# Kernel tuning notes

Hardware: AMD Instinct MI355X
Metric: run time of the kernel (lower is better)

Reference implementation:

```python
import jax, jax.numpy as jnp
import numpy as np

EPS_BN = 1e-5
K_DET = 50

def conv2d(x, w, b, pad):
    y = jax.lax.conv_general_dilated(x, w, (1, 1), [(pad, pad), (pad, pad)],
                                     dimension_numbers=('NCHW', 'OIHW', 'NCHW'))
    return y + b[None, :, None, None]

def branch2(x, w1, b1, w2, b2):
    # conv3x3 -> relu -> conv1x1
    return conv2d(jax.nn.relu(conv2d(x, w1, b1, 1)), w2, b2, 0)

def roi_head(x, w1, b1, g, beta, m, v, w2, b2):
    # conv3x3 -> BN(eval) -> relu -> global avg pool -> conv1x1
    h = conv2d(x, w1, b1, 1)
    h = (h - m[None, :, None, None]) * (g[None, :, None, None] / jnp.sqrt(v[None, :, None, None] + EPS_BN)) + beta[None, :, None, None]
    h = jax.nn.relu(h)
    h = jnp.mean(h, axis=(2, 3), keepdims=True)
    return conv2d(h, w2, b2, 0)[:, :, 0, 0]

def nms_hm(heat, kernel=3):
    pad = (kernel - 1) // 2
    hmax = jax.lax.reduce_window(heat, -jnp.inf, jax.lax.max,
                                 (1, 1, kernel, kernel), (1, 1, 1, 1),
                                 [(0, 0), (0, 0), (pad, pad), (pad, pad)])
    return heat * (hmax == heat).astype(heat.dtype)

def select_topk(heat, K):
    B, C, H, W = heat.shape
    s_all, i_all = jax.lax.top_k(heat.reshape(B, C, H * W), K)   # per-class topk
    scores, idx = jax.lax.top_k(s_all.reshape(B, C * K), K)      # overall topk
    classes = idx // K
    inds = jnp.take_along_axis(i_all.reshape(B, C * K), idx, axis=1)  # flat HW inds
    return scores, inds, classes

def roi_align_7x7(feat, boxes, sr=2):
    # torchvision roi_align, spatial_scale=1, aligned=False, sampling_ratio=sr
    B, C, H, W = feat.shape
    N = boxes.shape[0]
    b = boxes[:, 0].astype(jnp.int32)
    x1, y1, x2, y2 = boxes[:, 1], boxes[:, 2], boxes[:, 3], boxes[:, 4]
    roi_w = jnp.maximum(x2 - x1, 1.0)
    roi_h = jnp.maximum(y2 - y1, 1.0)
    bw = roi_w / 7.0
    bh = roi_h / 7.0
    S = 7 * sr
    off = (jnp.arange(S, dtype=feat.dtype) + 0.5) / sr  # sample offsets in bin units
    xs = x1[:, None] + bw[:, None] * off[None, :]       # (N,S)
    ys = y1[:, None] + bh[:, None] * off[None, :]
    X = jnp.broadcast_to(xs[:, None, :], (N, S, S))
    Y = jnp.broadcast_to(ys[:, :, None], (N, S, S))
    valid = (X > -1.0) & (X < W) & (Y > -1.0) & (Y < H)
    Xc = jnp.clip(X, 0.0, W - 1.0)
    Yc = jnp.clip(Y, 0.0, H - 1.0)
    x0 = jnp.floor(Xc).astype(jnp.int32)
    y0 = jnp.floor(Yc).astype(jnp.int32)
    x1i = jnp.minimum(x0 + 1, W - 1)
    y1i = jnp.minimum(y0 + 1, H - 1)
    lx = Xc - x0
    ly = Yc - y0
    flat = feat.transpose(0, 2, 3, 1).reshape(B * H * W, C)
    base = (b * H * W)[:, None, None]
    g = lambda yy, xx: flat[base + yy * W + xx]  # (N,S,S,C)
    v = (((1 - ly) * (1 - lx))[..., None] * g(y0, x0)
         + ((1 - ly) * lx)[..., None] * g(y0, x1i)
         + (ly * (1 - lx))[..., None] * g(y1i, x0)
         + (ly * lx)[..., None] * g(y1i, x1i))
    v = v * valid[..., None]
    v = v.reshape(N, 7, sr, 7, sr, C).mean(axis=(2, 4))
    return v.transpose(0, 3, 1, 2)  # (N,C,7,7)

def project_to_rect(calib, pts):
    c_u, c_v = calib[:, 0, 2], calib[:, 1, 2]
    f_u, f_v = calib[:, 0, 0], calib[:, 1, 1]
    b_x = calib[:, 0, 3] / (-f_u)
    b_y = calib[:, 1, 3] / (-f_v)
    x = (pts[:, 0] - c_u) * pts[:, 2] / f_u + b_x
    y = (pts[:, 1] - c_v) * pts[:, 2] / f_v + b_y
    return jnp.stack([x, y, pts[:, 2]], -1)

HEAD_NAMES = ['dep', 'o3', 's3', 'hd']

def setup_inputs():
    key = jax.random.key(0)
    ks = iter(jax.random.split(key, 64))
    B, Cin, H, W = 8, 64, 96, 320
    HC, NC = 256, 3
    f32 = jnp.float32
    rn = lambda shape, s=0.02: s * jax.random.normal(next(ks), shape, f32)
    inp = {}
    inp['features'] = jax.random.normal(next(ks), (B, Cin, H, W), f32)
    base = jnp.array([[700., 0., 640., 0.], [0., 700., 192., 0.], [0., 0., 1., 0.]], f32)
    inp['calib'] = base[None] + (jax.random.uniform(next(ks), (B, 3, 4), f32) - 0.5) * 2.0
    crb = jnp.array([[0., 0.], [1280., 384.]], f32)
    inp['coord_ranges'] = crb[None] + (jax.random.uniform(next(ks), (B, 2, 2), f32) - 0.5) * 2.0
    inp['mean_size'] = jnp.array([[3.88, 1.63, 1.53], [0.84, 0.66, 1.76], [1.76, 0.60, 1.73]], f32)
    inp['hm_w1'] = rn((HC, Cin, 3, 3)); inp['hm_b1'] = jnp.zeros(HC, f32)
    inp['hm_w2'] = rn((3, HC, 1, 1)); inp['hm_b2'] = jnp.full((3,), -np.log(1 / 0.1 - 1), f32)
    inp['o2_w1'] = rn((HC, Cin, 3, 3)); inp['o2_b1'] = jnp.zeros(HC, f32)
    inp['o2_w2'] = rn((2, HC, 1, 1)); inp['o2_b2'] = jnp.zeros(2, f32)
    inp['s2_w1'] = rn((HC, Cin, 3, 3)); inp['s2_b1'] = jnp.zeros(HC, f32)
    inp['s2_w2'] = rn((2, HC, 1, 1)); inp['s2_b2'] = 8.0 * jnp.ones(2, f32)
    Croi = Cin + 2 + NC
    for name, oc in zip(HEAD_NAMES, [2, 2, 4, 24]):
        inp[name + '_w1'] = rn((HC, Croi, 3, 3)); inp[name + '_b1'] = jnp.zeros(HC, f32)
        inp[name + '_g'] = 1.0 + 0.1 * jax.random.normal(next(ks), (HC,), f32)
        inp[name + '_beta'] = 0.1 * jax.random.normal(next(ks), (HC,), f32)
        inp[name + '_m'] = 0.1 * jax.random.normal(next(ks), (HC,), f32)
        inp[name + '_v'] = 1.0 + jax.random.uniform(next(ks), (HC,), f32)
        inp[name + '_w2'] = rn((oc, HC, 1, 1)); inp[name + '_b2'] = jnp.zeros(oc, f32)
    return inp

def reference(features, calib, coord_ranges, mean_size,
              hm_w1, hm_b1, hm_w2, hm_b2,
              o2_w1, o2_b1, o2_w2, o2_b2,
              s2_w1, s2_b1, s2_w2, s2_b2,
              dep_w1, dep_b1, dep_g, dep_beta, dep_m, dep_v, dep_w2, dep_b2,
              o3_w1, o3_b1, o3_g, o3_beta, o3_m, o3_v, o3_w2, o3_b2,
              s3_w1, s3_b1, s3_g, s3_beta, s3_m, s3_v, s3_w2, s3_b2,
              hd_w1, hd_b1, hd_g, hd_beta, hd_m, hd_v, hd_w2, hd_b2):
    B, Cf, H, W = features.shape
    dt = features.dtype
    heatmap = branch2(features, hm_w1, hm_b1, hm_w2, hm_b2)    # (B,3,H,W)
    offset_2d = branch2(features, o2_w1, o2_b1, o2_w2, o2_b2)  # (B,2,H,W)
    size_2d = branch2(features, s2_w1, s2_b1, s2_w2, s2_b2)    # (B,2,H,W)
    heat = nms_hm(heatmap)
    _, inds, classes = select_topk(heat, K_DET)                # (B,K)
    # coord map and box2d maps (B,5,H,W): [batch_idx, x1,y1,x2,y2]
    xs = jnp.arange(W, dtype=dt)
    ys = jnp.arange(H, dtype=dt)
    coord = jnp.stack([jnp.broadcast_to(xs[None, :], (H, W)),
                       jnp.broadcast_to(ys[:, None], (H, W))], 0)[None]
    center = coord + offset_2d
    bidx = jnp.broadcast_to(jnp.arange(B, dtype=dt)[:, None, None, None], (B, 1, H, W))
    box2d_maps = jnp.concatenate([bidx, center - size_2d / 2, center + size_2d / 2], 1)
    bm = box2d_maps.reshape(B, 5, H * W).transpose(0, 2, 1)    # (B,HW,5)
    boxes = jnp.take_along_axis(bm, inds[:, :, None], axis=1).reshape(-1, 5)  # (N,5)
    N = boxes.shape[0]
    roi_feat = roi_align_7x7(features, boxes)                  # (N,C,7,7)
    rb = boxes[:, 0].astype(jnp.int32)
    cr = coord_ranges[rb]                                      # (N,2,2)
    sx = cr[:, 1, 0] - cr[:, 0, 0]
    sy = cr[:, 1, 1] - cr[:, 0, 1]
    box_img = jnp.stack([boxes[:, 0],
                         boxes[:, 1] / W * sx + cr[:, 0, 0],
                         boxes[:, 2] / H * sy + cr[:, 0, 1],
                         boxes[:, 3] / W * sx + cr[:, 0, 0],
                         boxes[:, 4] / H * sy + cr[:, 0, 1]], -1)
    roi_calib = calib[rb]                                      # (N,3,4)
    ones = jnp.ones((N, 1), dt)
    p1 = project_to_rect(roi_calib, jnp.concatenate([box_img[:, 1:3], ones], -1))[:, :2]
    p2 = project_to_rect(roi_calib, jnp.concatenate([box_img[:, 3:5], ones], -1))[:, :2]
    t = jnp.arange(7, dtype=dt) / 6.0
    cx = p1[:, 0:1] + t[None, :] * (p2[:, 0:1] - p1[:, 0:1])   # (N,7)
    cy = p1[:, 1:2] + t[None, :] * (p2[:, 1:2] - p1[:, 1:2])
    coord_maps = jnp.stack([jnp.broadcast_to(cx[:, None, :], (N, 7, 7)),
                            jnp.broadcast_to(cy[:, :, None], (N, 7, 7))], 1)
    cls = classes.reshape(-1)
    NC = mean_size.shape[0]
    cls_hot = jax.nn.one_hot(cls, NC, dtype=dt)
    roi_in = jnp.concatenate([roi_feat, coord_maps,
                              jnp.broadcast_to(cls_hot[:, :, None, None], (N, NC, 7, 7))], 1)
    box2d_h = jnp.maximum(box_img[:, 4] - box_img[:, 2], 1.0)
    s3 = roi_head(roi_in, s3_w1, s3_b1, s3_g, s3_beta, s3_m, s3_v, s3_w2, s3_b2)  # (N,4)
    h3d_log_std = s3[:, 3:4]
    size3d_offset = s3[:, :3]
    size_3d = mean_size[cls] + size3d_offset
    f_u = roi_calib[:, 0, 0]
    depth_geo = size_3d[:, 0] / box2d_h * f_u
    dep = roi_head(roi_in, dep_w1, dep_b1, dep_g, dep_beta, dep_m, dep_v, dep_w2, dep_b2)
    depth_geo_log_std = (h3d_log_std[:, 0] + 2.0 * (jnp.log(f_u) - jnp.log(box2d_h)))[:, None]
    depth_log_std = jax.nn.logsumexp(jnp.concatenate([dep[:, 1:2], depth_geo_log_std], -1), axis=-1, keepdims=True)
    depth = jnp.concatenate([1.0 / (jax.nn.sigmoid(dep[:, 0:1]) + 1e-6) - 1.0 + depth_geo[:, None],
                             depth_log_std], -1)
    heading = roi_head(roi_in, hd_w1, hd_b1, hd_g, hd_beta, hd_m, hd_v, hd_w2, hd_b2)
    offset_3d = roi_head(roi_in, o3_w1, o3_b1, o3_g, o3_beta, o3_m, o3_v, o3_w2, o3_b2)
    return (heatmap, offset_2d, size_2d, heading, depth, offset_3d, size3d_offset, h3d_log_std)
```

## Files before the change

kernel.cpp:

```cpp
#include <hip/hip_runtime.h>
#include <math.h>

typedef unsigned short u16;
typedef unsigned int   u32;
typedef unsigned long long u64;
typedef __attribute__((ext_vector_type(8))) short short8;
typedef __attribute__((ext_vector_type(4))) float f32x4;

__device__ __forceinline__ float b2f(u16 v) { return __uint_as_float(((u32)v) << 16); }
__device__ __forceinline__ u16 f2b(float f) {
    u32 u = __float_as_uint(f);
    u32 r = (u + 0x7FFFu + ((u >> 16) & 1u)) >> 16;
    return (u16)r;
}
__device__ __forceinline__ float gload(const void* p, long i, int bf) {
    return bf ? b2f(((const u16*)p)[i]) : ((const float*)p)[i];
}
__device__ __forceinline__ void gstore(void* p, long i, float v, int bf) {
    if (bf) ((u16*)p)[i] = f2b(v);
    else    ((float*)p)[i] = v;
}

__device__ __forceinline__ u64 packKey(float v, int idx) {
    u32 u = __float_as_uint(v);
    u32 m = (u & 0x80000000u) ? ~u : (u | 0x80000000u);
    return ((u64)(~m) << 32) | (u32)idx;
}

__device__ int blockFlag(const void* feat) {
    __shared__ int fcnt;
    if (threadIdx.x == 0) fcnt = 0;
    __syncthreads();
    int sane = 0;
    for (int i = threadIdx.x; i < 512; i += blockDim.x) {
        u16 v = ((const u16*)feat)[i];
        float f = b2f(v);
        u32 e = (v >> 7) & 0xFF;
        float a = fabsf(f);
        sane += (e != 0xFF) && (f == 0.f || (a >= 1e-8f && a <= 1e4f));
    }
    atomicAdd(&fcnt, sane);
    __syncthreads();
    return fcnt >= 480;
}

#define BATCH 8
#define CIN   64
#define FH    96
#define FW    320
#define KDET  50
#define NROI  400
#define CROI  69
#define HW    (FH*FW)
#define CHUNK 1920
#define NCHUNK 16

#define WS_HEAT 0L
#define WS_OFF2 737280L
#define WS_SIZ2 1228800L
#define WS_NH   1720320L
#define WS_S1S  2457600L
#define WS_S1I  2458800L
#define WS_CLS  2460000L
#define WS_BOX  2460400L
#define WS_ROI  2462400L
#define WS_HOUT 3814800L
#define WS_W1T  3827600L
#define WS_WB16 3975056L
#define WS_W1H  4269968L
#define WS_PAR  4905872L
#define WS_FLAG 4938960L
#define WS_FEATT 4938964L
#define WS_END  (WS_FEATT + 7864320L)

#define PB_CAL 0
#define PB_CRN 96
#define PB_MSZ 128
#define PB_BR0 144
#define PB_HD0 3264

#define O_HEAT 0L
#define O_OFF2 737280L
#define O_SIZ2 1228800L
#define O_HEAD 1720320L
#define O_DEP  1729920L
#define O_OFF3 1730720L
#define O_S3D  1731520L
#define O_H3D  1732720L

struct WPtrs { const void* bw[3]; const void* hw[4]; };
struct Seg { const void* src; int n; int dst; };
struct Segs { Seg s[40]; int cnt; };

__global__ void kPrepWP(WPtrs P, Segs S, const void* __restrict__ feat,
                        int* __restrict__ flag, float* __restrict__ w1t,
                        u16* __restrict__ wb16, u16* __restrict__ whb,
                        float* __restrict__ par) {
    const int bf = blockFlag(feat);
    if (blockIdx.x == 0 && threadIdx.x == 0) *flag = bf;
    if (blockIdx.x < 5760) {
        int idx = blockIdx.x * 256 + threadIdx.x;
        if (idx < 147456) {
            int k = idx >> 8, c = idx & 255;
            w1t[idx] = gload(P.bw[0], (long)c * 576 + k, bf);
        } else if (idx < 589824) {
            int j = idx - 147456;
            int br = j / 147456, rem = j % 147456;
            int tap = rem / 16384;
            int r2 = rem & 16383;
            int s = r2 >> 13;
            int n = (r2 >> 5) & 255;
            int c5 = r2 & 31;
            int ci = s * 32 + c5;
            wb16[j] = f2b(gload(P.bw[br], (long)n * 576 + ci * 9 + tap, bf));
        } else {
            int j = idx - 589824;
            int h = j / 221184, rem = j % 221184;
            int tap = rem / 24576, rem2 = rem % 24576;
            int cs = rem2 / 8192, rem3 = rem2 % 8192;
            int oc = rem3 >> 5, jj = rem3 & 31;
            int ci = cs * 32 + jj;
            u16 val = 0;
            if (ci < CROI) val = f2b(gload(P.hw[h], (long)oc * 621 + ci * 9 + tap, bf));
            whb[j] = val;
        }
    } else {
        int sidx = blockIdx.x - 5760;
        if (sidx < S.cnt) {
            Seg sg = S.s[sidx];
            for (int i = threadIdx.x; i < sg.n; i += 256)
                par[sg.dst + i] = gload(sg.src, i, bf);
        }
    }
}

__global__ __launch_bounds__(256)
void kTrans(const void* __restrict__ feat, const int* __restrict__ flag,
            u16* __restrict__ featT) {
    __shared__ u16 t_lds[64][72];
    const int bf = *flag;
    const int x0 = blockIdx.x * 64, y = blockIdx.y, b = blockIdx.z;
    const int tid = threadIdx.x;
    for (int i = tid; i < 64 * 64; i += 256) {
        int c = i >> 6, x = i & 63;
        t_lds[x][c] = f2b(gload(feat, ((long)(b * CIN + c) * FH + y) * FW + x0 + x, bf));
    }
    __syncthreads();
    u16* outp = featT + (((long)b * FH + y) * FW + x0) * 64;
    for (int i = tid; i < 64 * 64; i += 256) {
        int x = i >> 6, c = i & 63;
        outp[(long)x * 64 + c] = t_lds[x][c];
    }
}

union MLds {
    struct { u16 a[4][68][72]; float red[8][64][3]; } c;
    struct {
        float in[4][3][36];
        union { float w[36 * 256]; float part[32 * 3 * 32]; } u;
    } s;
};

__global__ __launch_bounds__(512, 4)
void kBranch3M(const void* __restrict__ feat, const int* __restrict__ flag,
               const u16* __restrict__ wbAll,
               const float* __restrict__ bpAll,
               const float* __restrict__ w1t,
               void* __restrict__ outb, float* __restrict__ wsbase) {
    __shared__ __align__(16) MLds L;

    const long obase[3] = {O_HEAT, O_OFF2, O_SIZ2};
    const long wfs[3]   = {WS_HEAT, WS_OFF2, WS_SIZ2};

    const int bfl = *flag;
    const int tid = threadIdx.x;

    if (blockIdx.z == 8) {
        const int sidx = blockIdx.y * 5 + blockIdx.x;
        const int x0 = (sidx % 10) * 32;
        const int srem = sidx / 10;
        const int y = srem % 3;
        const int b = srem / 3;
        const float* bp = bpAll;
        const int OC = 3;
        const int xg = tid & 7, cg = tid >> 3;
        const int c0 = (cg & 31) * 8;

        float acc[8][4];
#pragma unroll
        for (int i = 0; i < 8; ++i)
#pragma unroll
            for (int j = 0; j < 4; ++j) acc[i][j] = 0.f;

        for (int chunk = 0; chunk < 16; ++chunk) {
            const int ci0 = chunk * 4;
            __syncthreads();
            for (int i = tid; i < 4 * 3 * 36; i += 512) {
                int xx = i % 36, t2 = i / 36;
                int r = t2 % 3, ci = t2 / 3;
                int gx = x0 - 1 + xx, gy = y - 1 + r;
                float v = 0.f;
                if (gx >= 0 && gx < FW && gy >= 0 && gy < FH)
                    v = gload(feat, ((long)(b * CIN + ci0 + ci) * FH + gy) * FW + gx, bfl);
                L.s.in[ci][r][xx] = v;
            }
            {
                const float4* src = (const float4*)(w1t + (long)ci0 * 9 * 256);
                float4* dst = (float4*)L.s.u.w;
                for (int i = tid; i < 36 * 256 / 4; i += 512) dst[i] = src[i];
            }
            __syncthreads();
            if (tid < 256) {
#pragma unroll
                for (int ci = 0; ci < 4; ++ci) {
#pragma unroll
                    for (int ky = 0; ky < 3; ++ky) {
                        const float* rowp = &L.s.in[ci][ky][xg * 4];
                        float inv[6];
                        *(float4*)&inv[0] = *(const float4*)&rowp[0];
                        *(float2*)&inv[4] = *(const float2*)&rowp[4];
#pragma unroll
                        for (int kx = 0; kx < 3; ++kx) {
                            const float* wp = &L.s.u.w[(ci * 9 + ky * 3 + kx) * 256 + c0];
                            float wv[8];
                            *(float4*)&wv[0] = *(const float4*)&wp[0];
                            *(float4*)&wv[4] = *(const float4*)&wp[4];
#pragma unroll
                            for (int cc = 0; cc < 8; ++cc)
#pragma unroll
                                for (int xx = 0; xx < 4; ++xx)
                                    acc[cc][xx] = fmaf(wv[cc], inv[xx + kx], acc[cc][xx]);
                        }
                    }
                }
            }
        }

        if (tid < 256) {
#pragma unroll
            for (int cc = 0; cc < 8; ++cc) {
                float b1v = bp[c0 + cc];
#pragma unroll
                for (int xx = 0; xx < 4; ++xx)
                    acc[cc][xx] = fmaxf(acc[cc][xx] + b1v, 0.f);
            }
        }
        __syncthreads();
        if (tid < 256) {
#pragma unroll
            for (int k = 0; k < OC; ++k) {
                float p[4];
#pragma unroll
                for (int xx = 0; xx < 4; ++xx) p[xx] = 0.f;
#pragma unroll
                for (int cc = 0; cc < 8; ++cc) {
                    float wv = bp[256 + k * 256 + c0 + cc];
#pragma unroll
                    for (int xx = 0; xx < 4; ++xx) p[xx] = fmaf(acc[cc][xx], wv, p[xx]);
                }
#pragma unroll
                for (int xx = 0; xx < 4; ++xx)
                    L.s.u.part[((cg & 31) * OC + k) * 32 + xg * 4 + xx] = p[xx];
            }
        }
        __syncthreads();
        float* outf = wsbase + WS_HEAT;
        for (int t = tid; t < OC * 32; t += 512) {
            int k = t >> 5, xx = t & 31;
            float s = bp[256 + OC * 256 + k];
#pragma unroll 8
            for (int g = 0; g < 32; ++g) s += L.s.u.part[(g * OC + k) * 32 + xx];
            long o = (((long)b * OC + k) * FH + y) * FW + x0 + xx;
            gstore(outb, O_HEAT + o, s, bfl);
            outf[o] = s;
        }
        return;
    }

    const int wave = tid >> 6, lane = tid & 63;
    const int q = lane >> 4, n15 = lane & 15;
    const int mg = wave >> 2, ng = wave & 3;
    const int x0 = blockIdx.x * 64, y0 = blockIdx.y * 2;
    const int b = blockIdx.z;

    if (tid < 256) {
        const int ci = tid & 63, rr = tid >> 6;
        const int gy = y0 - 1 + rr;
        if (gy < 0 || gy >= FH) {
            for (int xi = 0; xi < 66; ++xi) L.c.a[rr][xi][ci] = 0;
        } else if (bfl) {
            const u16* rp = (const u16*)feat + ((long)((b << 6) | ci) * FH + gy) * FW;
            for (int j = 0; j < 10; ++j) {
                int xs0 = x0 - 8 + j * 8;
                u16 tmp[8];
                if (xs0 >= 0 && xs0 <= FW - 8)
                    *(uint4*)tmp = *(const uint4*)(rp + xs0);
                else
                    for (int e = 0; e < 8; ++e) {
                        int gx = xs0 + e;
                        tmp[e] = (gx >= 0 && gx < FW) ? rp[gx] : (u16)0;
                    }
                for (int e = 0; e < 8; ++e) {
                    int xi = xs0 + e - x0 + 1;
                    if (xi >= 0 && xi < 66) L.c.a[rr][xi][ci] = tmp[e];
                }
            }
        } else {
            const float* rp = (const float*)feat + ((long)((b << 6) | ci) * FH + gy) * FW;
            for (int j = 0; j < 18; ++j) {
                int xs0 = x0 - 4 + j * 4;
                float tmp[4];
                if (xs0 >= 0 && xs0 <= FW - 4)
                    *(float4*)tmp = *(const float4*)(rp + xs0);
                else
                    for (int e = 0; e < 4; ++e) {
                        int gx = xs0 + e;
                        tmp[e] = (gx >= 0 && gx < FW) ? rp[gx] : 0.f;
                    }
                for (int e = 0; e < 4; ++e) {
                    int xi = xs0 + e - x0 + 1;
                    if (xi >= 0 && xi < 66) L.c.a[rr][xi][ci] = f2b(tmp[e]);
                }
            }
        }
    }
    __syncthreads();

#pragma unroll 1
    for (int br = 0; br < 3; ++br) {
        const int oc = (br == 0) ? 3 : 2;
        const u16* wpt = wbAll + br * 147456;
        const float* bp = bpAll + br * 1040;

        f32x4 acc[4][4];
#pragma unroll
        for (int i = 0; i < 4; ++i)
#pragma unroll
            for (int t = 0; t < 4; ++t) acc[i][t] = (f32x4){0.f, 0.f, 0.f, 0.f};

#pragma unroll 1
        for (int tap = 0; tap < 9; ++tap) {
            const int ky = tap / 3, kx = tap % 3;
#pragma unroll
            for (int s = 0; s < 2; ++s) {
                const u16* wks = wpt + (tap * 2 + s) * 8192;
                short8 bfr[4];
#pragma unroll
                for (int t = 0; t < 4; ++t)
                    bfr[t] = *(const short8*)(wks + (ng * 64 + t * 16 + n15) * 32 + q * 8);
                short8 afr[4];
#pragma unroll
                for (int i = 0; i < 4; ++i)
                    afr[i] = *(const short8*)&L.c.a[mg + ky][i * 16 + n15 + kx][s * 32 + q * 8];
#pragma unroll
                for (int i = 0; i < 4; ++i)
#pragma unroll
                    for (int t = 0; t < 4; ++t)
                        acc[i][t] = __builtin_amdgcn_mfma_f32_16x16x32_bf16(
                            afr[i], bfr[t], acc[i][t], 0, 0, 0);
            }
        }

        float b1v[4], w2v[3][4];
#pragma unroll
        for (int t = 0; t < 4; ++t) {
            int n = ng * 64 + t * 16 + n15;
            b1v[t] = bp[n];
#pragma unroll
            for (int k = 0; k < 3; ++k) w2v[k][t] = bp[256 + k * 256 + n];
        }
        __syncthreads();
#pragma unroll
        for (int i = 0; i < 4; ++i) {
#pragma unroll
            for (int r = 0; r < 4; ++r) {
                float pk[3];
#pragma unroll
                for (int k = 0; k < 3; ++k) pk[k] = 0.f;
#pragma unroll
                for (int t = 0; t < 4; ++t) {
                    float h = fmaxf(acc[i][t][r] + b1v[t], 0.f);
#pragma unroll
                    for (int k = 0; k < 3; ++k) pk[k] = fmaf(h, w2v[k][t], pk[k]);
                }
#pragma unroll
                for (int k = 0; k < 3; ++k) {
                    pk[k] += __shfl_xor(pk[k], 1);
                    pk[k] += __shfl_xor(pk[k], 2);
                    pk[k] += __shfl_xor(pk[k], 4);
                    pk[k] += __shfl_xor(pk[k], 8);
                }
                if (n15 == 0) {
                    int ml = i * 16 + q * 4 + r;
#pragma unroll
                    for (int k = 0; k < 3; ++k) L.c.red[wave][ml][k] = pk[k];
                }
            }
        }
        __syncthreads();
        float* outf = wsbase + wfs[br];
        for (int t2 = tid; t2 < oc * 128; t2 += 512) {
            int k = t2 >> 7, m = t2 & 127;
            int row = m >> 6, x = m & 63;
            int mg2 = m >> 6, ml = m & 63;
            float s = bp[256 + oc * 256 + k];
#pragma unroll
            for (int w = 0; w < 4; ++w) s += L.c.red[mg2 * 4 + w][ml][k];
            int grow = y0 + row;
            if (br == 0 && grow < 3) continue;
            long o = (((long)b * oc + k) * FH + grow) * FW + x0 + x;
            gstore(outb, obase[br] + o, s, bfl);
            outf[o] = s;
        }
    }
}

__global__ __launch_bounds__(256)
void kNmsTopA(const float* __restrict__ heat, float* __restrict__ nh) {
    __shared__ float hrow[8][320];
    __shared__ u64 keys[CHUNK];
    const int bc = blockIdx.x, ch = blockIdx.y;
    const int tid = threadIdx.x;
    const int r0 = ch * 6;
    const float* hp = heat + (long)bc * HW;

    for (int i = tid; i < 8 * 320; i += 256) {
        int rr = i / 320, x = i % 320;
        int gy = r0 - 1 + rr;
        hrow[rr][x] = (gy >= 0 && gy < FH) ? hp[(long)gy * FW + x] : -INFINITY;
    }
    __syncthreads();
    for (int i = tid; i < CHUNK; i += 256) {
        int ry = i / 320, x = i % 320;
        float v = hrow[ry + 1][x];
        float m = v;
        int xm = max(x - 1, 0), xp = min(x + 1, FW - 1);
#pragma unroll
        for (int dy = 0; dy < 3; ++dy) {
            m = fmaxf(m, hrow[ry + dy][xm]);
            m = fmaxf(m, hrow[ry + dy][x]);
            m = fmaxf(m, hrow[ry + dy][xp]);
        }
        float nv = (v == m) ? v : 0.f;
        keys[i] = packKey(nv, ch * CHUNK + i);
    }
    __syncthreads();
    if (tid < 64) {
        const int lane = tid;
        u64* outp = (u64*)(nh + (long)bc * HW + (long)ch * CHUNK);
        for (int it = 0; it < KDET; ++it) {
            u64 bk = ~0ULL; int bp = 0;
            for (int i = lane; i < CHUNK; i += 64) {
                u64 k = keys[i];
                if (k < bk) { bk = k; bp = i; }
            }
#pragma unroll
            for (int s = 32; s > 0; s >>= 1) {
                u64 k2 = __shfl_down(bk, s);
                int p2 = __shfl_down(bp, s);
                if (k2 < bk) { bk = k2; bp = p2; }
            }
            bk = __shfl(bk, 0);
            bp = __shfl(bp, 0);
            if (lane == 0) {
                outp[it] = bk;
                keys[bp] = ~0ULL;
            }
        }
    }
}

__global__ __launch_bounds__(192)
void kTopBC(const float* __restrict__ nh, const float* __restrict__ off2,
            const float* __restrict__ siz2, float* __restrict__ boxes,
            int* __restrict__ clsArr) {
    __shared__ u64 keys[3][NCHUNK * KDET];
    __shared__ float sc[150];
    __shared__ int   si[150];
    const int b = blockIdx.x, tid = threadIdx.x;
    const int wave = tid >> 6, lane = tid & 63;
    const int bc = b * 3 + wave;

    for (int ch = 0; ch < NCHUNK; ++ch) {
        const u64* src = (const u64*)(nh + (long)bc * HW + (long)ch * CHUNK);
        if (lane < KDET) keys[wave][ch * KDET + lane] = src[lane];
    }
    __syncthreads();
    for (int it = 0; it < KDET; ++it) {
        u64 bk = ~0ULL; int bp = 0;
        for (int i = lane; i < NCHUNK * KDET; i += 64) {
            u64 k = keys[wave][i];
            if (k < bk) { bk = k; bp = i; }
        }
#pragma unroll
        for (int s = 32; s > 0; s >>= 1) {
            u64 k2 = __shfl_down(bk, s);
            int p2 = __shfl_down(bp, s);
            if (k2 < bk) { bk = k2; bp = p2; }
        }
        bk = __shfl(bk, 0);
        bp = __shfl(bp, 0);
        if (lane == 0) {
            u32 hm = ~(u32)(bk >> 32);
            u32 u = (hm & 0x80000000u) ? (hm & 0x7fffffffu) : ~hm;
            sc[wave * KDET + it] = __uint_as_float(u);
            si[wave * KDET + it] = (int)(bk & 0xFFFFFFFFu);
            keys[wave][bp] = ~0ULL;
        }
    }
    __syncthreads();
    if (wave == 0) {
        const int t = lane;
        for (int r = 0; r < KDET; ++r) {
            float bv = -INFINITY; int bp = 0x7fffffff;
            for (int i = t; i < 150; i += 64) {
                float v = sc[i];
                if (v > bv) { bv = v; bp = i; }
            }
#pragma unroll
            for (int s = 32; s > 0; s >>= 1) {
                float v2 = __shfl_down(bv, s);
                int   p2 = __shfl_down(bp, s);
                if (v2 > bv || (v2 == bv && p2 < bp)) { bv = v2; bp = p2; }
            }
            bp = __shfl(bp, 0);
            if (t == 0) {
                int cls = bp / KDET;
                int ind = si[bp];
                int n = b * KDET + r;
                clsArr[n] = cls;
                int x = ind % FW, yy = ind / FW;
                float cx = (float)x  + off2[(((long)b * 2 + 0) * FH + yy) * FW + x];
                float cy = (float)yy + off2[(((long)b * 2 + 1) * FH + yy) * FW + x];
                float w  = siz2[(((long)b * 2 + 0) * FH + yy) * FW + x];
                float h  = siz2[(((long)b * 2 + 1) * FH + yy) * FW + x];
                boxes[n * 5 + 0] = (float)b;
                boxes[n * 5 + 1] = cx - w * 0.5f;
                boxes[n * 5 + 2] = cy - h * 0.5f;
                boxes[n * 5 + 3] = cx + w * 0.5f;
                boxes[n * 5 + 4] = cy + h * 0.5f;
                sc[bp] = -INFINITY;
            }
        }
    }
}

#define ROI_META \
    if (tid < 14) { \
        float roi_w = fmaxf(bx2 - bx1, 1.f); \
        float X = bx1 + (roi_w / 7.f) * ((tid + 0.5f) * 0.5f); \
        vxs[tid] = (X > -1.f) && (X < (float)FW); \
        float Xc = fminf(fmaxf(X, 0.f), (float)(FW - 1)); \
        int xi = (int)floorf(Xc); \
        x0s[tid] = xi; x1s[tid] = min(xi + 1, FW - 1); lxs[tid] = Xc - (float)xi; \
    } else if (tid >= 16 && tid < 30) { \
        int i = tid - 16; \
        float roi_h = fmaxf(by2 - by1, 1.f); \
        float Y = by1 + (roi_h / 7.f) * ((i + 0.5f) * 0.5f); \
        vys[i] = (Y > -1.f) && (Y < (float)FH); \
        float Yc = fminf(fmaxf(Y, 0.f), (float)(FH - 1)); \
        int yi = (int)floorf(Yc); \
        y0s[i] = yi; y1s[i] = min(yi + 1, FH - 1); lys[i] = Yc - (float)yi; \
    } else if (tid >= 32 && tid < 46) { \
        int j = tid - 32; \
        const float* cal = par + PB_CAL + b * 12; \
        float f_u = cal[0], c_u = cal[2], t03 = cal[3]; \
        float f_v = cal[5], c_v = cal[6], t13 = cal[7]; \
        float bxc = t03 / (-f_u), byc = t13 / (-f_v); \
        const float* cr = par + PB_CRN + b * 4; \
        float crx0 = cr[0], cry0 = cr[1], crx1 = cr[2], cry1 = cr[3]; \
        float sx = crx1 - crx0, sy = cry1 - cry0; \
        float u1 = bx1 / (float)FW * sx + crx0, v1 = by1 / (float)FH * sy + cry0; \
        float u2 = bx2 / (float)FW * sx + crx0, v2 = by2 / (float)FH * sy + cry0; \
        float p1x = (u1 - c_u) / f_u + bxc, p1y = (v1 - c_v) / f_v + byc; \
        float p2x = (u2 - c_u) / f_u + bxc, p2y = (v2 - c_v) / f_v + byc; \
        if (j < 7) cxs[j] = p1x + ((float)j / 6.f) * (p2x - p1x); \
        else       cys[j - 7] = p1y + ((float)(j - 7) / 6.f) * (p2y - p1y); \
    }

__global__ __launch_bounds__(256)
void kRoiT(const u16* __restrict__ featT, const float* __restrict__ boxes,
           const int* __restrict__ clsArr, const float* __restrict__ par,
           float* __restrict__ roi_in) {
    const int n = blockIdx.x, tid = threadIdx.x;
    __shared__ int   x0s[14], x1s[14], y0s[14], y1s[14], vxs[14], vys[14];
    __shared__ float lxs[14], lys[14], cxs[7], cys[7];

    const float bx1 = boxes[n * 5 + 1], by1 = boxes[n * 5 + 2];
    const float bx2 = boxes[n * 5 + 3], by2 = boxes[n * 5 + 4];
    const int b = (int)boxes[n * 5 + 0];

    ROI_META
    __syncthreads();

    const u16* fb = featT + (long)b * FH * FW * 64;
    for (int t = tid; t < CIN * 49; t += 256) {
        int c = t & 63, p = t >> 6;
        int oy = p / 7, ox = p % 7;
        float acc = 0.f;
#pragma unroll
        for (int dy = 0; dy < 2; ++dy) {
            int sy = oy * 2 + dy;
            float ly = lys[sy]; int yA = y0s[sy], yB = y1s[sy], vy = vys[sy];
#pragma unroll
            for (int dx = 0; dx < 2; ++dx) {
                int sx = ox * 2 + dx;
                float lx = lxs[sx]; int xA = x0s[sx], xB = x1s[sx];
                float v = (1.f - ly) * (1.f - lx) * b2f(fb[((long)yA * FW + xA) * 64 + c])
                        + (1.f - ly) * lx         * b2f(fb[((long)yA * FW + xB) * 64 + c])
                        + ly * (1.f - lx)         * b2f(fb[((long)yB * FW + xA) * 64 + c])
                        + ly * lx                 * b2f(fb[((long)yB * FW + xB) * 64 + c]);
                if (!(vy && vxs[sx])) v = 0.f;
                acc += v;
            }
        }
        roi_in[((long)n * CROI + c) * 49 + p] = acc * 0.25f;
    }
    int cls = clsArr[n];
    for (int t = tid; t < 5 * 49; t += 256) {
        int ch = t / 49, p = t % 49, i = p / 7, j = p % 7;
        float v;
        if (ch == 0)      v = cxs[j];
        else if (ch == 1) v = cys[i];
        else              v = (cls == ch - 2) ? 1.f : 0.f;
        roi_in[((long)n * CROI + 64 + ch) * 49 + p] = v;
    }
}

__global__ __launch_bounds__(256)
void kRoi(const void* __restrict__ feat, const int* __restrict__ flag,
          const float* __restrict__ boxes, const int* __restrict__ clsArr,
          const float* __restrict__ par, float* __restrict__ roi_in) {
    const int n = blockIdx.x, tid = threadIdx.x;
    const int bf = *flag;
    __shared__ int   x0s[14], x1s[14], y0s[14], y1s[14], vxs[14], vys[14];
    __shared__ float lxs[14], lys[14], cxs[7], cys[7];

    const float bx1 = boxes[n * 5 + 1], by1 = boxes[n * 5 + 2];
    const float bx2 = boxes[n * 5 + 3], by2 = boxes[n * 5 + 4];
    const int b = (int)boxes[n * 5 + 0];

    ROI_META
    __syncthreads();

    for (int t = tid; t < CIN * 49; t += 256) {
        int c = t / 49, p = t % 49, oy = p / 7, ox = p % 7;
        long fb = ((long)b * CIN + c) * HW;
        float acc = 0.f;
#pragma unroll
        for (int dy = 0; dy < 2; ++dy) {
            int sy = oy * 2 + dy;
            float ly = lys[sy]; int yA = y0s[sy], yB = y1s[sy], vy = vys[sy];
#pragma unroll
            for (int dx = 0; dx < 2; ++dx) {
                int sx = ox * 2 + dx;
                float lx = lxs[sx]; int xA = x0s[sx], xB = x1s[sx];
                float v = (1.f - ly) * (1.f - lx) * gload(feat, fb + yA * FW + xA, bf)
                        + (1.f - ly) * lx         * gload(feat, fb + yA * FW + xB, bf)
                        + ly * (1.f - lx)         * gload(feat, fb + yB * FW + xA, bf)
                        + ly * lx                 * gload(feat, fb + yB * FW + xB, bf);
                if (!(vy && vxs[sx])) v = 0.f;
                acc += v;
            }
        }
        roi_in[((long)n * CROI + c) * 49 + p] = acc * 0.25f;
    }
    int cls = clsArr[n];
    for (int t = tid; t < 5 * 49; t += 256) {
        int ch = t / 49, p = t % 49, i = p / 7, j = p % 7;
        float v;
        if (ch == 0)      v = cxs[j];
        else if (ch == 1) v = cys[i];
        else              v = (cls == ch - 2) ? 1.f : 0.f;
        roi_in[((long)n * CROI + 64 + ch) * 49 + p] = v;
    }
}

__global__ __launch_bounds__(256, 4)
void kHeadM(const float* __restrict__ roi_in, const u16* __restrict__ whb,
            const float* __restrict__ par, float* __restrict__ head_out) {
    const int h = blockIdx.x, n = blockIdx.y, tid = threadIdx.x;
    const int wave = tid >> 6, lane = tid & 63;
    const int q = lane >> 4, n15 = lane & 15;
    const int ocArr[4] = {2, 2, 4, 24};
    const int offArr[4] = {0, 2, 4, 8};
    __shared__ __align__(16) u16 r_lds[9][9][104];
    __shared__ float means[256];

    for (int i = tid; i < 9 * 9 * 104 / 8; i += 256)
        ((uint4*)r_lds)[i] = (uint4){0, 0, 0, 0};
    __syncthreads();
    const float* rp = roi_in + (long)n * CROI * 49;
    for (int i = tid; i < CROI * 49; i += 256) {
        int c = i / 49, p = i % 49;
        r_lds[p / 7 + 1][p % 7 + 1][c] = f2b(rp[i]);
    }
    __syncthreads();

    int oyA[4], oxA[4];
#pragma unroll
    for (int i = 0; i < 4; ++i) {
        int pos = i * 16 + n15; if (pos > 48) pos = 48;
        oyA[i] = pos / 7; oxA[i] = pos % 7;
    }

    f32x4 acc[4][4];
#pragma unroll
    for (int i = 0; i < 4; ++i)
#pragma unroll
        for (int t = 0; t < 4; ++t) acc[i][t] = (f32x4){0.f, 0.f, 0.f, 0.f};

#pragma unroll 1
    for (int tap = 0; tap < 9; ++tap) {
        const int ky = tap / 3, kx = tap % 3;
        const u16* wt = whb + ((long)h * 9 + tap) * 24576;
#pragma unroll
        for (int cs = 0; cs < 3; ++cs) {
            short8 afr[4], bfr[4];
#pragma unroll
            for (int i = 0; i < 4; ++i)
                afr[i] = *(const short8*)&r_lds[oyA[i] + ky][oxA[i] + kx][cs * 32 + q * 8];
#pragma unroll
            for (int t = 0; t < 4; ++t)
                bfr[t] = *(const short8*)(wt + ((cs << 8) + wave * 64 + t * 16 + n15) * 32 + q * 8);
#pragma unroll
            for (int i = 0; i < 4; ++i)
#pragma unroll
                for (int t = 0; t < 4; ++t)
                    acc[i][t] = __builtin_amdgcn_mfma_f32_16x16x32_bf16(
                        afr[i], bfr[t], acc[i][t], 0, 0, 0);
        }
    }

    const float* hb = par + PB_HD0 + h * 7456;
#pragma unroll
    for (int t = 0; t < 4; ++t) {
        int oc = wave * 64 + t * 16 + n15;
        float b1 = hb[oc], g = hb[256 + oc], be = hb[512 + oc];
        float m = hb[768 + oc], v = hb[1024 + oc];
        float scale = g / sqrtf(v + 1e-5f);
        float s = 0.f;
#pragma unroll
        for (int i = 0; i < 4; ++i)
#pragma unroll
            for (int r = 0; r < 4; ++r) {
                int pos = i * 16 + q * 4 + r;
                if (pos < 49)
                    s += fmaxf((acc[i][t][r] + b1 - m) * scale + be, 0.f);
            }
        s += __shfl_xor(s, 16);
        s += __shfl_xor(s, 32);
        if (q == 0) means[oc] = s / 49.f;
    }
    __syncthreads();

    int oc_out = ocArr[h];
    const float* w2 = hb + 1280;
    for (int k = wave; k < oc_out; k += 4) {
        float s = 0.f;
        for (int c = lane; c < 256; c += 64) s += means[c] * w2[k * 256 + c];
#pragma unroll
        for (int off = 32; off > 0; off >>= 1) s += __shfl_down(s, off);
        if (lane == 0)
            head_out[(long)n * 32 + offArr[h] + k] = s + w2[oc_out * 256 + k];
    }
}

__global__ void kFinal(const float* __restrict__ head_out, const float* __restrict__ boxes,
                       const int* __restrict__ clsArr, const float* __restrict__ par,
                       void* __restrict__ out, const int* __restrict__ flag) {
    int n = blockIdx.x * 256 + threadIdx.x;
    if (n >= NROI) return;
    const int bf = *flag;
    const float* ho = head_out + (long)n * 32;
    float dep0 = ho[0], dep1 = ho[1];
    int b = (int)boxes[n * 5 + 0];
    int cls = clsArr[n];

    for (int j = 0; j < 24; ++j) gstore(out, O_HEAD + n * 24 + j, ho[8 + j], bf);
    gstore(out, O_OFF3 + n * 2 + 0, ho[2], bf);
    gstore(out, O_OFF3 + n * 2 + 1, ho[3], bf);
    gstore(out, O_S3D + n * 3 + 0, ho[4], bf);
    gstore(out, O_S3D + n * 3 + 1, ho[5], bf);
    gstore(out, O_S3D + n * 3 + 2, ho[6], bf);
    gstore(out, O_H3D + n, ho[7], bf);

    float cry0 = par[PB_CRN + b * 4 + 1], cry1 = par[PB_CRN + b * 4 + 3];
    float sy = cry1 - cry0;
    float bi2 = boxes[n * 5 + 2] / (float)FH * sy + cry0;
    float bi4 = boxes[n * 5 + 4] / (float)FH * sy + cry0;
    float box_h = fmaxf(bi4 - bi2, 1.f);
    float f_u = par[PB_CAL + b * 12 + 0];
    float size3d0 = par[PB_MSZ + cls * 3 + 0] + ho[4];
    float depth_geo = size3d0 / box_h * f_u;
    float sig = 1.f / (1.f + expf(-dep0));
    float d0 = 1.f / (sig + 1e-6f) - 1.f + depth_geo;
    float dgls = ho[7] + 2.f * (logf(f_u) - logf(box_h));
    float mx = fmaxf(dep1, dgls);
    float lse = mx + logf(expf(dep1 - mx) + expf(dgls - mx));
    gstore(out, O_DEP + n * 2 + 0, d0, bf);
    gstore(out, O_DEP + n * 2 + 1, lse, bf);
}

extern "C" void kernel_launch(void* const* d_in, const int* in_sizes, int n_in,
                              void* d_out, int out_size, void* d_ws, size_t ws_size,
                              hipStream_t stream) {
    (void)in_sizes; (void)n_in; (void)out_size;
    float* ws = (float*)d_ws;
    float* par = ws + WS_PAR;
    int* flag = (int*)(ws + WS_FLAG);
    u16* wb16 = (u16*)(ws + WS_WB16);
    u16* whb  = (u16*)(ws + WS_W1H);
    u16* featT = (u16*)(ws + WS_FEATT);
    const void* feat = d_in[0];
    const bool bigws = ws_size >= (size_t)WS_END * 4;

    WPtrs WP;
    WP.bw[0] = d_in[4]; WP.bw[1] = d_in[8]; WP.bw[2] = d_in[12];
    WP.hw[0] = d_in[16]; WP.hw[1] = d_in[24]; WP.hw[2] = d_in[32]; WP.hw[3] = d_in[40];

    Segs SG; int si = 0;
    auto add = [&](const void* s, int n, int dst) {
        SG.s[si].src = s; SG.s[si].n = n; SG.s[si].dst = dst; ++si;
    };
    add(d_in[1], 96, PB_CAL); add(d_in[2], 32, PB_CRN); add(d_in[3], 9, PB_MSZ);
    const int ocb[3] = {3, 2, 2};
    for (int b = 0; b < 3; ++b) {
        int base = PB_BR0 + b * 1040;
        int i0 = 4 + 4 * b;
        add(d_in[i0 + 1], 256, base);
        add(d_in[i0 + 2], ocb[b] * 256, base + 256);
        add(d_in[i0 + 3], ocb[b], base + 256 + ocb[b] * 256);
    }
    const int och[4] = {2, 2, 4, 24};
    for (int h = 0; h < 4; ++h) {
        int base = PB_HD0 + h * 7456;
        int i0 = 16 + 8 * h;
        add(d_in[i0 + 1], 256, base);
        add(d_in[i0 + 2], 256, base + 256);
        add(d_in[i0 + 3], 256, base + 512);
        add(d_in[i0 + 4], 256, base + 768);
        add(d_in[i0 + 5], 256, base + 1024);
        add(d_in[i0 + 6], och[h] * 256, base + 1280);
        add(d_in[i0 + 7], och[h], base + 1280 + och[h] * 256);
    }
    SG.cnt = si;

    kPrepWP<<<5760 + 40, 256, 0, stream>>>(WP, SG, feat, flag,
                                           ws + WS_W1T, wb16, whb, par);
    if (bigws)
        kTrans<<<dim3(5, 96, 8), 256, 0, stream>>>(feat, flag, featT);

    kBranch3M<<<dim3(5, 48, 9), 512, 0, stream>>>(
        feat, flag, wb16, par + PB_BR0, ws + WS_W1T, d_out, ws);

    kNmsTopA<<<dim3(24, NCHUNK), 256, 0, stream>>>(ws + WS_HEAT, ws + WS_NH);
    kTopBC<<<8, 192, 0, stream>>>(ws + WS_NH, ws + WS_OFF2, ws + WS_SIZ2,
                                  ws + WS_BOX, (int*)(ws + WS_CLS));
    if (bigws)
        kRoiT<<<400, 256, 0, stream>>>(featT, ws + WS_BOX, (int*)(ws + WS_CLS),
                                       par, ws + WS_ROI);
    else
        kRoi<<<400, 256, 0, stream>>>(feat, flag, ws + WS_BOX, (int*)(ws + WS_CLS),
                                      par, ws + WS_ROI);
    kHeadM<<<dim3(4, NROI), 256, 0, stream>>>(ws + WS_ROI, whb, par, ws + WS_HOUT);
    kFinal<<<2, 256, 0, stream>>>(ws + WS_HOUT, ws + WS_BOX, (int*)(ws + WS_CLS),
                                  par, d_out, flag);
}
```

Baseline: 802.8 us.

## Fuse transpose into branch kernel, fuse ROI align into heads, parallelize NMS top-k

The feature transpose now runs as an extra z-slice of the branch conv kernel rather than as a separate launch, so it can overlap with the conv blocks. ROI align is fused into the head MFMA kernel, which samples straight into LDS and skips the roi_in round trip through global memory. The cost is that ROI sampling is repeated for each of the four heads. The per-chunk top-50 selection now uses four waves, each taking a top-50 over its 480 keys, followed by a merge pass in one wave, which shortens the serial selection loop.

```diff
diff --git a/kernel.cpp b/kernel.cpp
--- a/kernel.cpp
+++ b/kernel.cpp
@@ -59,8 +59,6 @@
 #define WS_OFF2 737280L
 #define WS_SIZ2 1228800L
 #define WS_NH   1720320L
-#define WS_S1S  2457600L
-#define WS_S1I  2458800L
 #define WS_CLS  2460000L
 #define WS_BOX  2460400L
 #define WS_ROI  2462400L
@@ -134,31 +132,13 @@
     }
 }
 
-__global__ __launch_bounds__(256)
-void kTrans(const void* __restrict__ feat, const int* __restrict__ flag,
-            u16* __restrict__ featT) {
-    __shared__ u16 t_lds[64][72];
-    const int bf = *flag;
-    const int x0 = blockIdx.x * 64, y = blockIdx.y, b = blockIdx.z;
-    const int tid = threadIdx.x;
-    for (int i = tid; i < 64 * 64; i += 256) {
-        int c = i >> 6, x = i & 63;
-        t_lds[x][c] = f2b(gload(feat, ((long)(b * CIN + c) * FH + y) * FW + x0 + x, bf));
-    }
-    __syncthreads();
-    u16* outp = featT + (((long)b * FH + y) * FW + x0) * 64;
-    for (int i = tid; i < 64 * 64; i += 256) {
-        int x = i >> 6, c = i & 63;
-        outp[(long)x * 64 + c] = t_lds[x][c];
-    }
-}
-
 union MLds {
     struct { u16 a[4][68][72]; float red[8][64][3]; } c;
     struct {
         float in[4][3][36];
         union { float w[36 * 256]; float part[32 * 3 * 32]; } u;
     } s;
+    u16 t[64][72];
 };
 
 __global__ __launch_bounds__(512, 4)
@@ -174,6 +154,27 @@
 
     const int bfl = *flag;
     const int tid = threadIdx.x;
+
+    if (blockIdx.z == 9) {
+        u16* featT = (u16*)(wsbase + WS_FEATT);
+        const int x0 = blockIdx.x * 64;
+        const int y0 = blockIdx.y * 2;
+        for (int sub = 0; sub < 16; ++sub) {
+            const int b = sub >> 1, y = y0 + (sub & 1);
+            __syncthreads();
+            for (int i = tid; i < 64 * 64; i += 512) {
+                int c = i >> 6, x = i & 63;
+                L.t[x][c] = f2b(gload(feat, ((long)(b * CIN + c) * FH + y) * FW + x0 + x, bfl));
+            }
+            __syncthreads();
+            u16* outp = featT + (((long)b * FH + y) * FW + x0) * 64;
+            for (int i = tid; i < 64 * 64; i += 512) {
+                int x = i >> 6, c = i & 63;
+                outp[(long)x * 64 + c] = L.t[x][c];
+            }
+        }
+        return;
+    }
 
     if (blockIdx.z == 8) {
         const int sidx = blockIdx.y * 5 + blockIdx.x;
@@ -419,8 +420,10 @@
 void kNmsTopA(const float* __restrict__ heat, float* __restrict__ nh) {
     __shared__ float hrow[8][320];
     __shared__ u64 keys[CHUNK];
+    __shared__ u64 sub[4][KDET];
     const int bc = blockIdx.x, ch = blockIdx.y;
     const int tid = threadIdx.x;
+    const int wave = tid >> 6, lane = tid & 63;
     const int r0 = ch * 6;
     const float* hp = heat + (long)bc * HW;
 
@@ -445,13 +448,12 @@
         keys[i] = packKey(nv, ch * CHUNK + i);
     }
     __syncthreads();
-    if (tid < 64) {
-        const int lane = tid;
-        u64* outp = (u64*)(nh + (long)bc * HW + (long)ch * CHUNK);
+    {
+        u64* kw = keys + wave * 480;
         for (int it = 0; it < KDET; ++it) {
             u64 bk = ~0ULL; int bp = 0;
-            for (int i = lane; i < CHUNK; i += 64) {
-                u64 k = keys[i];
+            for (int i = lane; i < 480; i += 64) {
+                u64 k = kw[i];
                 if (k < bk) { bk = k; bp = i; }
             }
 #pragma unroll
@@ -463,8 +465,32 @@
             bk = __shfl(bk, 0);
             bp = __shfl(bp, 0);
             if (lane == 0) {
+                sub[wave][it] = bk;
+                kw[bp] = ~0ULL;
+            }
+        }
+    }
+    __syncthreads();
+    if (wave == 0) {
+        u64* outp = (u64*)(nh + (long)bc * HW + (long)ch * CHUNK);
+        u64* sp = &sub[0][0];
+        for (int it = 0; it < KDET; ++it) {
+            u64 bk = ~0ULL; int bp = 0;
+            for (int i = lane; i < 4 * KDET; i += 64) {
+                u64 k = sp[i];
+                if (k < bk) { bk = k; bp = i; }
+            }
+#pragma unroll
+            for (int s = 32; s > 0; s >>= 1) {
+                u64 k2 = __shfl_down(bk, s);
+                int p2 = __shfl_down(bp, s);
+                if (k2 < bk) { bk = k2; bp = p2; }
+            }
+            bk = __shfl(bk, 0);
+            bp = __shfl(bp, 0);
+            if (lane == 0) {
                 outp[it] = bk;
-                keys[bp] = ~0ULL;
+                sp[bp] = ~0ULL;
             }
         }
     }
@@ -578,19 +604,27 @@
         else       cys[j - 7] = p1y + ((float)(j - 7) / 6.f) * (p2y - p1y); \
     }
 
-__global__ __launch_bounds__(256)
-void kRoiT(const u16* __restrict__ featT, const float* __restrict__ boxes,
-           const int* __restrict__ clsArr, const float* __restrict__ par,
-           float* __restrict__ roi_in) {
-    const int n = blockIdx.x, tid = threadIdx.x;
+__global__ __launch_bounds__(256, 4)
+void kHeadM2(const u16* __restrict__ featT, const float* __restrict__ boxes,
+             const int* __restrict__ clsArr, const u16* __restrict__ whb,
+             const float* __restrict__ par, float* __restrict__ head_out) {
+    const int h = blockIdx.x, n = blockIdx.y, tid = threadIdx.x;
+    const int wave = tid >> 6, lane = tid & 63;
+    const int q = lane >> 4, n15 = lane & 15;
+    const int ocArr[4] = {2, 2, 4, 24};
+    const int offArr[4] = {0, 2, 4, 8};
+    __shared__ __align__(16) u16 r_lds[9][9][104];
+    __shared__ float means[256];
     __shared__ int   x0s[14], x1s[14], y0s[14], y1s[14], vxs[14], vys[14];
     __shared__ float lxs[14], lys[14], cxs[7], cys[7];
 
     const float bx1 = boxes[n * 5 + 1], by1 = boxes[n * 5 + 2];
     const float bx2 = boxes[n * 5 + 3], by2 = boxes[n * 5 + 4];
     const int b = (int)boxes[n * 5 + 0];
-
     ROI_META
+
+    for (int i = tid; i < 9 * 9 * 104 / 8; i += 256)
+        ((uint4*)r_lds)[i] = (uint4){0, 0, 0, 0};
     __syncthreads();
 
     const u16* fb = featT + (long)b * FH * FW * 64;
@@ -614,16 +648,87 @@
                 acc += v;
             }
         }
-        roi_in[((long)n * CROI + c) * 49 + p] = acc * 0.25f;
-    }
-    int cls = clsArr[n];
-    for (int t = tid; t < 5 * 49; t += 256) {
-        int ch = t / 49, p = t % 49, i = p / 7, j = p % 7;
-        float v;
-        if (ch == 0)      v = cxs[j];
-        else if (ch == 1) v = cys[i];
-        else              v = (cls == ch - 2) ? 1.f : 0.f;
-        roi_in[((long)n * CROI + 64 + ch) * 49 + p] = v;
+        r_lds[oy + 1][ox + 1][c] = f2b(acc * 0.25f);
+    }
+    {
+        int cls = clsArr[n];
+        for (int t = tid; t < 5 * 49; t += 256) {
+            int ch = t / 49, p = t % 49, i = p / 7, j = p % 7;
+            float v;
+            if (ch == 0)      v = cxs[j];
+            else if (ch == 1) v = cys[i];
+            else              v = (cls == ch - 2) ? 1.f : 0.f;
+            r_lds[i + 1][j + 1][64 + ch] = f2b(v);
+        }
+    }
+    __syncthreads();
+
+    int oyA[4], oxA[4];
+#pragma unroll
+    for (int i = 0; i < 4; ++i) {
+        int pos = i * 16 + n15; if (pos > 48) pos = 48;
+        oyA[i] = pos / 7; oxA[i] = pos % 7;
+    }
+
+    f32x4 acc[4][4];
+#pragma unroll
+    for (int i = 0; i < 4; ++i)
+#pragma unroll
+        for (int t = 0; t < 4; ++t) acc[i][t] = (f32x4){0.f, 0.f, 0.f, 0.f};
+
+#pragma unroll 1
+    for (int tap = 0; tap < 9; ++tap) {
+        const int ky = tap / 3, kx = tap % 3;
+        const u16* wt = whb + ((long)h * 9 + tap) * 24576;
+#pragma unroll
+        for (int cs = 0; cs < 3; ++cs) {
+            short8 afr[4], bfr[4];
+#pragma unroll
+            for (int i = 0; i < 4; ++i)
+                afr[i] = *(const short8*)&r_lds[oyA[i] + ky][oxA[i] + kx][cs * 32 + q * 8];
+#pragma unroll
+            for (int t = 0; t < 4; ++t)
+                bfr[t] = *(const short8*)(wt + ((cs << 8) + wave * 64 + t * 16 + n15) * 32 + q * 8);
+#pragma unroll
+            for (int i = 0; i < 4; ++i)
+#pragma unroll
+                for (int t = 0; t < 4; ++t)
+                    acc[i][t] = __builtin_amdgcn_mfma_f32_16x16x32_bf16(
+                        afr[i], bfr[t], acc[i][t], 0, 0, 0);
+        }
+    }
+
+    const float* hb = par + PB_HD0 + h * 7456;
+#pragma unroll
+    for (int t = 0; t < 4; ++t) {
+        int oc = wave * 64 + t * 16 + n15;
+        float b1 = hb[oc], g = hb[256 + oc], be = hb[512 + oc];
+        float m = hb[768 + oc], v = hb[1024 + oc];
+        float scale = g / sqrtf(v + 1e-5f);
+        float s = 0.f;
+#pragma unroll
+        for (int i = 0; i < 4; ++i)
+#pragma unroll
+            for (int r = 0; r < 4; ++r) {
+                int pos = i * 16 + q * 4 + r;
+                if (pos < 49)
+                    s += fmaxf((acc[i][t][r] + b1 - m) * scale + be, 0.f);
+            }
+        s += __shfl_xor(s, 16);
+        s += __shfl_xor(s, 32);
+        if (q == 0) means[oc] = s / 49.f;
+    }
+    __syncthreads();
+
+    int oc_out = ocArr[h];
+    const float* w2 = hb + 1280;
+    for (int k = wave; k < oc_out; k += 4) {
+        float s = 0.f;
+        for (int c = lane; c < 256; c += 64) s += means[c] * w2[k * 256 + c];
+#pragma unroll
+        for (int off = 32; off > 0; off >>= 1) s += __shfl_down(s, off);
+        if (lane == 0)
+            head_out[(long)n * 32 + offArr[h] + k] = s + w2[oc_out * 256 + k];
     }
 }
 
@@ -848,22 +953,22 @@
 
     kPrepWP<<<5760 + 40, 256, 0, stream>>>(WP, SG, feat, flag,
                                            ws + WS_W1T, wb16, whb, par);
-    if (bigws)
-        kTrans<<<dim3(5, 96, 8), 256, 0, stream>>>(feat, flag, featT);
-
-    kBranch3M<<<dim3(5, 48, 9), 512, 0, stream>>>(
+
+    kBranch3M<<<dim3(5, 48, bigws ? 10 : 9), 512, 0, stream>>>(
         feat, flag, wb16, par + PB_BR0, ws + WS_W1T, d_out, ws);
 
     kNmsTopA<<<dim3(24, NCHUNK), 256, 0, stream>>>(ws + WS_HEAT, ws + WS_NH);
     kTopBC<<<8, 192, 0, stream>>>(ws + WS_NH, ws + WS_OFF2, ws + WS_SIZ2,
                                   ws + WS_BOX, (int*)(ws + WS_CLS));
-    if (bigws)
-        kRoiT<<<400, 256, 0, stream>>>(featT, ws + WS_BOX, (int*)(ws + WS_CLS),
-                                       par, ws + WS_ROI);
-    else
+    if (bigws) {
+        kHeadM2<<<dim3(4, NROI), 256, 0, stream>>>(featT, ws + WS_BOX,
+                                                   (int*)(ws + WS_CLS), whb, par,
+                                                   ws + WS_HOUT);
+    } else {
         kRoi<<<400, 256, 0, stream>>>(feat, flag, ws + WS_BOX, (int*)(ws + WS_CLS),
                                       par, ws + WS_ROI);
-    kHeadM<<<dim3(4, NROI), 256, 0, stream>>>(ws + WS_ROI, whb, par, ws + WS_HOUT);
+        kHeadM<<<dim3(4, NROI), 256, 0, stream>>>(ws + WS_ROI, whb, par, ws + WS_HOUT);
+    }
     kFinal<<<2, 256, 0, stream>>>(ws + WS_HOUT, ws + WS_BOX, (int*)(ws + WS_CLS),
                                   par, d_out, flag);
 }
```

After: 747.3 us. 6.9% less time.
